# Performance work log

Measured on AMD Instinct MI355X. Metric: run time of the kernel, lower is better.

Reference implementation:

```python
import jax, jax.numpy as jnp
import numpy as np

N = 100000      # nodes
E = 1600000     # edges
G = 2048        # graphs
IN_DIM = 32
PEP_DIM = 768
H = 64          # hidden_dim
L = 3           # num_layers
BN_EPS = 1e-5


def setup_inputs() -> dict:
    key = jax.random.key(0)
    ks = jax.random.split(key, 32)
    x = jax.random.normal(ks[0], (N, IN_DIM), dtype=jnp.float32)
    edge_index = jax.random.randint(ks[1], (2, E), 0, N, dtype=jnp.int32)
    batch_idx = jnp.sort(jax.random.randint(ks[2], (N,), 0, G, dtype=jnp.int32))
    edge_attr = jax.random.normal(ks[3], (E, 2), dtype=jnp.float32)
    peptide_emb = jax.random.normal(ks[4], (G, PEP_DIM), dtype=jnp.float32)
    s = 0.1
    p = {
        'in_w': jax.random.normal(ks[5], (IN_DIM, H)) * s,
        'in_b': jnp.zeros((H,)),
        'e_w': jax.random.normal(ks[6], (2, H)) * s,
        'e_b': jnp.zeros((H,)),
        'conv_w1': jax.random.normal(ks[7], (L, H, H)) * s,
        'conv_b1': jnp.zeros((L, H)),
        'conv_w2': jax.random.normal(ks[8], (L, H, H)) * s,
        'conv_b2': jnp.zeros((L, H)),
        'bn_w': jnp.ones((L, H)),
        'bn_b': jnp.zeros((L, H)),
        'bn_mean': jnp.zeros((L, H)),
        'bn_var': jnp.ones((L, H)),
        'vn_w1': jax.random.normal(ks[9], (H, H)) * s,
        'vn_b1': jnp.zeros((H,)),
        'vn_w2': jax.random.normal(ks[10], (H, H)) * s,
        'vn_b2': jnp.zeros((H,)),
        'pep_w': jax.random.normal(ks[11], (PEP_DIM, H)) * s,
        'pep_b': jnp.zeros((H,)),
        'cls_w1': jax.random.normal(ks[12], (2 * H, H)) * s,
        'cls_b1': jnp.zeros((H,)),
        'cls_w2': jax.random.normal(ks[13], (H, 1)) * s,
        'cls_b2': jnp.zeros((1,)),
    }
    out = {'x': x, 'edge_index': edge_index, 'batch_idx': batch_idx,
           'edge_attr': edge_attr, 'peptide_emb': peptide_emb}
    out.update(p)
    return out


def reference(x, edge_index, batch_idx, edge_attr, peptide_emb,
              in_w, in_b, e_w, e_b,
              conv_w1, conv_b1, conv_w2, conv_b2,
              bn_w, bn_b, bn_mean, bn_var,
              vn_w1, vn_b1, vn_w2, vn_b2,
              pep_w, pep_b, cls_w1, cls_b1, cls_w2, cls_b2):
    seg = jax.ops.segment_sum
    src, dst = edge_index[0], edge_index[1]

    h = x @ in_w + in_b                       # [N,H]
    e = edge_attr @ e_w + e_b                 # [E,H]
    vn = jnp.zeros((G, H), dtype=h.dtype)     # virtual node per graph

    for i in range(L):
        h = h + vn[batch_idx]
        # GINE conv: (1+eps)*h + sum_j relu(h_j + e_ji), eps=0
        msg = jax.nn.relu(h[src] + e)                 # [E,H]
        agg = seg(msg, dst, num_segments=N)           # scatter-add to targets
        z = h + agg
        m = jax.nn.relu(z @ conv_w1[i] + conv_b1[i]) @ conv_w2[i] + conv_b2[i]
        # BatchNorm (eval: running stats)
        m = (m - bn_mean[i]) * jax.lax.rsqrt(bn_var[i] + BN_EPS) * bn_w[i] + bn_b[i]
        h = jax.nn.relu(m)                            # dropout = identity (eval)
        if i != L - 1:
            pooled = seg(h, batch_idx, num_segments=G)
            vn = vn + (jax.nn.relu(pooled @ vn_w1 + vn_b1) @ vn_w2 + vn_b2)

    # mean pooling
    counts = seg(jnp.ones((N,), dtype=h.dtype), batch_idx, num_segments=G)
    graph_emb = seg(h, batch_idx, num_segments=G) / jnp.maximum(counts, 1.0)[:, None]

    pep_hidden = jax.nn.relu(peptide_emb @ pep_w + pep_b)  # dropout = identity
    fused = jnp.concatenate([graph_emb, pep_hidden], axis=1)  # [G,2H]
    logits = (jax.nn.relu(fused @ cls_w1 + cls_b1) @ cls_w2 + cls_b2).reshape(-1)
    return logits
```

## Files before the change

kernel.cpp:

```cpp
#include <hip/hip_runtime.h>

#define NN 100000
#define NE 1600000
#define NG 2048
#define IN_DIM 32
#define PEP_DIM 768
#define H 64
#define BN_EPS 1e-5f
#define CONV_W 16
#define NGRP (NN / CONV_W)
#define GATHER_BLOCKS 512
#define NTILE ((NN + 63) / 64)
#define MLP_BLOCKS 512
#define BUCK_SHIFT 9
#define NBUCK ((NN + 511) >> 9)
#define NBLKA 256
#define CHUNK ((NE + NBLKA - 1) / NBLKA)

typedef unsigned int uint;
typedef unsigned short ushort;
typedef __attribute__((ext_vector_type(8))) __bf16 bf16x8;
typedef __attribute__((ext_vector_type(4))) float f32x4;

__device__ __forceinline__ float bf2f(uint u) {
    return __uint_as_float((u & 0xFFFFu) << 16);
}
__device__ __forceinline__ uint f2bf(float x) {
    uint b = __float_as_uint(x);
    return (b + 0x7FFFu + ((b >> 16) & 1u)) >> 16;
}


__global__ __launch_bounds__(256) void k_hist(const int* __restrict__ ei, int* __restrict__ mat) {
    __shared__ int hloc[NBUCK];
    for (int i = threadIdx.x; i < NBUCK; i += 256) hloc[i] = 0;
    __syncthreads();
    int base = blockIdx.x * CHUNK;
    int end = min(NE, base + CHUNK);
    for (int e = base + threadIdx.x; e < end; e += 256)
        atomicAdd(&hloc[ei[NE + e] >> BUCK_SHIFT], 1);
    __syncthreads();
    for (int i = threadIdx.x; i < NBUCK; i += 256)
        mat[i * NBLKA + blockIdx.x] = hloc[i];
}

__global__ __launch_bounds__(NBLKA) void k_s1(int* __restrict__ mat, int* __restrict__ tot) {
    __shared__ int s[NBLKA];
    int b = blockIdx.x;
    int v = mat[b * NBLKA + threadIdx.x];
    s[threadIdx.x] = v;
    __syncthreads();
    for (int off = 1; off < NBLKA; off <<= 1) {
        int x = (threadIdx.x >= off) ? s[threadIdx.x - off] : 0;
        __syncthreads();
        s[threadIdx.x] += x;
        __syncthreads();
    }
    mat[b * NBLKA + threadIdx.x] = s[threadIdx.x] - v;
    if (threadIdx.x == NBLKA - 1) tot[b] = s[threadIdx.x];
}

__global__ __launch_bounds__(256) void k_s2(const int* __restrict__ tot, int* __restrict__ bases) {
    __shared__ int s[256];
    int v = (threadIdx.x < NBUCK) ? tot[threadIdx.x] : 0;
    s[threadIdx.x] = v;
    __syncthreads();
    for (int off = 1; off < 256; off <<= 1) {
        int x = (threadIdx.x >= off) ? s[threadIdx.x - off] : 0;
        __syncthreads();
        s[threadIdx.x] += x;
        __syncthreads();
    }
    if (threadIdx.x < NBUCK) bases[threadIdx.x] = s[threadIdx.x] - v;
    if (threadIdx.x == 255) bases[NBUCK] = s[255];
}

__global__ __launch_bounds__(256) void k_scat1(const int* __restrict__ ei, const float* __restrict__ ea,
                                               const int* __restrict__ mat, const int* __restrict__ bases,
                                               int2* __restrict__ tmp) {
    __shared__ int cur[NBUCK];
    for (int i = threadIdx.x; i < NBUCK; i += 256)
        cur[i] = bases[i] + mat[i * NBLKA + blockIdx.x];
    __syncthreads();
    int base = blockIdx.x * CHUNK;
    int end = min(NE, base + CHUNK);
    for (int e = base + threadIdx.x; e < end; e += 256) {
        int dst = ei[NE + e];
        int bk = dst >> BUCK_SHIFT;
        int pos = atomicAdd(&cur[bk], 1);
        float2 a = *(const float2*)(ea + (size_t)e * 2);
        int2 r;
        r.x = ei[e] | ((dst & 511) << 17);
        r.y = (int)(f2bf(a.x) | (f2bf(a.y) << 16));
        tmp[pos] = r;
    }
}

__global__ __launch_bounds__(256) void k_scat2(const int2* __restrict__ tmp, const int* __restrict__ bases,
                                               int2* __restrict__ csr, int* __restrict__ row_start) {
    __shared__ int deg[512];
    __shared__ int psc[256];
    __shared__ int cur[512];
    int b = blockIdx.x;
    int t = threadIdx.x;
    int s0 = bases[b], s1 = bases[b + 1];
    deg[2 * t] = 0; deg[2 * t + 1] = 0;
    __syncthreads();
    for (int e = s0 + t; e < s1; e += 256)
        atomicAdd(&deg[(tmp[e].x >> 17) & 511], 1);
    __syncthreads();
    int d0 = deg[2 * t], d1 = deg[2 * t + 1];
    psc[t] = d0 + d1;
    __syncthreads();
    for (int off = 1; off < 256; off <<= 1) {
        int x = (t >= off) ? psc[t - off] : 0;
        __syncthreads();
        psc[t] += x;
        __syncthreads();
    }
    int ep = psc[t] - (d0 + d1);
    int node0 = (b << BUCK_SHIFT) + 2 * t;
    int e0 = s0 + ep, e1 = e0 + d0;
    cur[2 * t] = e0; cur[2 * t + 1] = e1;
    if (node0 < NN) row_start[node0] = e0;
    if (node0 + 1 < NN) row_start[node0 + 1] = e1;
    __syncthreads();
    for (int e = s0 + t; e < s1; e += 256) {
        int2 r = tmp[e];
        int nl = (r.x >> 17) & 511;
        int pos = atomicAdd(&cur[nl], 1);
        int2 o;
        o.x = r.x & 0x1FFFF;
        o.y = r.y;
        csr[pos] = o;
    }
    if (b == NBUCK - 1 && t == 0) row_start[NN] = NE;
}

__global__ void k_gstart(const int* __restrict__ batch, int* __restrict__ gstart) {
    int i = blockIdx.x * 256 + threadIdx.x;
    if (i >= NN) return;
    int b = batch[i];
    int p = (i == 0) ? -1 : batch[i - 1];
    for (int g = p + 1; g <= b; g++) gstart[g] = i;
    if (i == NN - 1) {
        for (int g = b + 1; g <= NG; g++) gstart[g] = NN;
    }
}

__global__ void k_init_h(const float* __restrict__ x, const float* __restrict__ w,
                         const float* __restrict__ b, ushort* __restrict__ h) {
    int t = blockIdx.x * 256 + threadIdx.x;
    int node = t >> 4;
    if (node >= NN) return;
    int c4 = (t & 15) * 4;
    float4 acc = *(const float4*)(b + c4);
    const float* xr = x + node * IN_DIM;
    for (int k = 0; k < IN_DIM; k++) {
        float xv = xr[k];
        float4 wv = *(const float4*)(w + k * H + c4);
        acc.x += xv * wv.x; acc.y += xv * wv.y;
        acc.z += xv * wv.z; acc.w += xv * wv.w;
    }
    uint2 o;
    o.x = f2bf(acc.x) | (f2bf(acc.y) << 16);
    o.y = f2bf(acc.z) | (f2bf(acc.w) << 16);
    *(uint2*)(h + (size_t)node * H + c4) = o;
}

__global__ void k_prep(const float* __restrict__ w1, const float* __restrict__ w2,
                       ushort* __restrict__ wp) {
    int t = blockIdx.x * 256 + threadIdx.x;
    if (t >= 3 * 8192) return;
    int j = t & 7;
    int lane = (t >> 3) & 63;
    int ct = (t >> 9) & 3;
    int ks = (t >> 11) & 1;
    int st = (t >> 12) & 1;
    int ly = t >> 13;
    int k = ks * 32 + (lane >> 4) * 8 + j;
    int c = ct * 16 + (lane & 15);
    const float* src = (st == 0) ? w1 : w2;
    wp[t] = (ushort)f2bf(src[ly * H * H + k * H + c]);
}

__global__ __launch_bounds__(1024, 4) void k_gather(
    const ushort* __restrict__ h_in, ushort* __restrict__ z,
    const int2* __restrict__ csr, const int* __restrict__ row_start,
    const float* __restrict__ ew, const float* __restrict__ eb) {
    int w = threadIdx.x >> 6;
    int c = threadIdx.x & 63;
    float ew0 = ew[c], ew1 = ew[H + c], ebc = eb[c];
    for (int grp = blockIdx.x; grp < NGRP; grp += GATHER_BLOCKS) {
        int node = grp * CONV_W + w;
        int rs = __builtin_amdgcn_readfirstlane(row_start[node]);
        int re = __builtin_amdgcn_readfirstlane(row_start[node + 1]);
        float acc = 0.f;
        int j = rs;
        for (; j + 16 <= re; j += 16) {
            int2 v[16];
            #pragma unroll
            for (int t = 0; t < 16; t++) v[t] = csr[j + t];
            float hh[16];
            #pragma unroll
            for (int t = 0; t < 16; t++) hh[t] = bf2f(h_in[(size_t)v[t].x * H + c]);
            #pragma unroll
            for (int t = 0; t < 16; t++)
                acc += fmaxf(hh[t] + fmaf(bf2f(v[t].y), ew0, fmaf(bf2f((uint)v[t].y >> 16), ew1, ebc)), 0.f);
        }
        for (; j + 4 <= re; j += 4) {
            int2 v[4];
            #pragma unroll
            for (int t = 0; t < 4; t++) v[t] = csr[j + t];
            float hh[4];
            #pragma unroll
            for (int t = 0; t < 4; t++) hh[t] = bf2f(h_in[(size_t)v[t].x * H + c]);
            #pragma unroll
            for (int t = 0; t < 4; t++)
                acc += fmaxf(hh[t] + fmaf(bf2f(v[t].y), ew0, fmaf(bf2f((uint)v[t].y >> 16), ew1, ebc)), 0.f);
        }
        for (; j < re; j++) {
            int2 v = csr[j];
            float hs = bf2f(h_in[(size_t)v.x * H + c]);
            acc += fmaxf(hs + fmaf(bf2f(v.y), ew0, fmaf(bf2f((uint)v.y >> 16), ew1, ebc)), 0.f);
        }
        float zv = bf2f(h_in[(size_t)node * H + c]) + acc;
        uint me = f2bf(zv);
        uint nb2 = __shfl_down(me, 1, 64);
        if ((c & 1) == 0) {
            *(uint*)(z + (size_t)node * H + c) = me | (nb2 << 16);
        }
    }
}

__global__ __launch_bounds__(256, 4) void k_mlp(
    const ushort* __restrict__ z, ushort* __restrict__ h_out,
    const ushort* __restrict__ wp,
    const float* __restrict__ b1, const float* __restrict__ b2,
    const float* __restrict__ bnw, const float* __restrict__ bnb,
    const float* __restrict__ bnm, const float* __restrict__ bnv) {
    __shared__ ushort ts[4][16][72];
    int w = threadIdx.x >> 6;
    int l = threadIdx.x & 63;
    int r = l & 15;
    int kg = l >> 4;
    bf16x8 W1B0[4], W1B1[4], W2B0[4], W2B1[4];
    #pragma unroll
    for (int ct = 0; ct < 4; ct++) {
        W1B0[ct] = *(const bf16x8*)(wp + (0 * 4 + ct) * 512 + l * 8);
        W1B1[ct] = *(const bf16x8*)(wp + (1 * 4 + ct) * 512 + l * 8);
        W2B0[ct] = *(const bf16x8*)(wp + 4096 + (0 * 4 + ct) * 512 + l * 8);
        W2B1[ct] = *(const bf16x8*)(wp + 4096 + (1 * 4 + ct) * 512 + l * 8);
    }
    for (int tile = blockIdx.x; tile < NTILE; tile += MLP_BLOCKS) {
        int nb = tile * 64 + w * 16;
        if (nb >= NN) continue;
        const ushort* zr = z + (size_t)(nb + r) * H + kg * 8;
        bf16x8 A0 = *(const bf16x8*)(zr);
        bf16x8 A1 = *(const bf16x8*)(zr + 32);
        f32x4 acc[4];
        #pragma unroll
        for (int ct = 0; ct < 4; ct++) {
            f32x4 a = {0.f, 0.f, 0.f, 0.f};
            a = __builtin_amdgcn_mfma_f32_16x16x32_bf16(A0, W1B0[ct], a, 0, 0, 0);
            a = __builtin_amdgcn_mfma_f32_16x16x32_bf16(A1, W1B1[ct], a, 0, 0, 0);
            acc[ct] = a;
        }
        #pragma unroll
        for (int ct = 0; ct < 4; ct++) {
            int col = ct * 16 + r;
            float bb = b1[col];
            #pragma unroll
            for (int q = 0; q < 4; q++) {
                float tv = fmaxf(acc[ct][q] + bb, 0.f);
                ts[w][kg * 4 + q][col] = (ushort)f2bf(tv);
            }
        }
        bf16x8 T0 = *(const bf16x8*)(&ts[w][r][kg * 8]);
        bf16x8 T1 = *(const bf16x8*)(&ts[w][r][32 + kg * 8]);
        f32x4 acc2[4];
        #pragma unroll
        for (int ct = 0; ct < 4; ct++) {
            f32x4 a = {0.f, 0.f, 0.f, 0.f};
            a = __builtin_amdgcn_mfma_f32_16x16x32_bf16(T0, W2B0[ct], a, 0, 0, 0);
            a = __builtin_amdgcn_mfma_f32_16x16x32_bf16(T1, W2B1[ct], a, 0, 0, 0);
            acc2[ct] = a;
        }
        #pragma unroll
        for (int ct = 0; ct < 4; ct++) {
            int col = ct * 16 + r;
            float bb2 = b2[col];
            float mean = bnm[col];
            float sc = bnw[col] * rsqrtf(bnv[col] + BN_EPS);
            float bo = bnb[col];
            #pragma unroll
            for (int q = 0; q < 4; q++) {
                float hv = fmaxf((acc2[ct][q] + bb2 - mean) * sc + bo, 0.f);
                ts[w][kg * 4 + q][col] = (ushort)f2bf(hv);
            }
        }
        #pragma unroll
        for (int it = 0; it < 4; it++) {
            int flat = it * 64 + l;
            int node = flat >> 4;
            int ch4 = (flat & 15) * 4;
            uint2 val = *(uint2*)(&ts[w][node][ch4]);
            *(uint2*)(h_out + (size_t)(nb + node) * H + ch4) = val;
        }
    }
}

__global__ __launch_bounds__(256) void k_poolvn(ushort* __restrict__ h,
                                                const int* __restrict__ gstart,
                                                float* __restrict__ pooled,
                                                const float* __restrict__ w1, const float* __restrict__ b1,
                                                const float* __restrict__ w2, const float* __restrict__ b2,
                                                float* __restrict__ vn, int do_vn) {
    __shared__ float ps[4][H];
    __shared__ float ts[4][H];
    int w = threadIdx.x >> 6, c = threadIdx.x & 63;
    int g = blockIdx.x * 4 + w;
    int s = __builtin_amdgcn_readfirstlane(gstart[g]);
    int e = __builtin_amdgcn_readfirstlane(gstart[g + 1]);
    float acc = 0.f;
    int n = s;
    for (; n + 4 <= e; n += 4) {
        float x0 = bf2f(h[(size_t)(n + 0) * H + c]);
        float x1 = bf2f(h[(size_t)(n + 1) * H + c]);
        float x2 = bf2f(h[(size_t)(n + 2) * H + c]);
        float x3 = bf2f(h[(size_t)(n + 3) * H + c]);
        acc += x0; acc += x1; acc += x2; acc += x3;
    }
    for (; n < e; n++) acc += bf2f(h[(size_t)n * H + c]);
    pooled[(size_t)g * H + c] = acc;
    if (!do_vn) return;
    ps[w][c] = acc;
    float a1 = b1[c];
    for (int k = 0; k < H; k += 4) {
        float4 pv = *(const float4*)&ps[w][k];
        a1 = fmaf(pv.x, w1[(k + 0) * H + c], a1);
        a1 = fmaf(pv.y, w1[(k + 1) * H + c], a1);
        a1 = fmaf(pv.z, w1[(k + 2) * H + c], a1);
        a1 = fmaf(pv.w, w1[(k + 3) * H + c], a1);
    }
    ts[w][c] = fmaxf(a1, 0.f);
    float a2 = b2[c];
    for (int k = 0; k < H; k += 4) {
        float4 tv = *(const float4*)&ts[w][k];
        a2 = fmaf(tv.x, w2[(k + 0) * H + c], a2);
        a2 = fmaf(tv.y, w2[(k + 1) * H + c], a2);
        a2 = fmaf(tv.z, w2[(k + 2) * H + c], a2);
        a2 = fmaf(tv.w, w2[(k + 3) * H + c], a2);
    }
    float vnew = vn[(size_t)g * H + c] + a2;
    vn[(size_t)g * H + c] = vnew;
    ps[w][c] = vnew;
    float vlo = ps[w][(c & 31) * 2 + 0];
    float vhi = ps[w][(c & 31) * 2 + 1];
    int ch2 = (c & 31) * 2;
    for (n = s; n + 2 <= e; n += 2) {
        size_t off = (size_t)(n + (c >> 5)) * H + ch2;
        uint u = *(uint*)(h + off);
        float lo = bf2f(u) + vlo;
        float hi = bf2f(u >> 16) + vhi;
        *(uint*)(h + off) = f2bf(lo) | (f2bf(hi) << 16);
    }
    if (n < e && c < 32) {
        size_t off = (size_t)n * H + ch2;
        uint u = *(uint*)(h + off);
        float lo = bf2f(u) + vlo;
        float hi = bf2f(u >> 16) + vhi;
        *(uint*)(h + off) = f2bf(lo) | (f2bf(hi) << 16);
    }
}

__global__ __launch_bounds__(256) void k_final(const float* __restrict__ pooled,
                                               const int* __restrict__ gstart,
                                               const float* __restrict__ pep,
                                               const float* __restrict__ pw, const float* __restrict__ pb,
                                               const float* __restrict__ cw1, const float* __restrict__ cb1,
                                               const float* __restrict__ cw2, const float* __restrict__ cb2,
                                               float* __restrict__ out) {
    __shared__ float red[4][H];
    __shared__ float fused[2 * H];
    int g = blockIdx.x;
    int lane = threadIdx.x & 63;
    int part = threadIdx.x >> 6;
    const float* pr = pep + (size_t)g * PEP_DIM;
    float acc = 0.0f;
    int k0 = part * (PEP_DIM / 4);
    for (int k = k0; k < k0 + PEP_DIM / 4; k++) {
        acc += pr[k] * pw[k * H + lane];
    }
    red[part][lane] = acc;
    __syncthreads();
    if (part == 0) {
        float s = red[0][lane] + red[1][lane] + red[2][lane] + red[3][lane] + pb[lane];
        fused[H + lane] = fmaxf(s, 0.0f);
        float c = (float)(gstart[g + 1] - gstart[g]);
        float invc = 1.0f / fmaxf(c, 1.0f);
        fused[lane] = pooled[(size_t)g * H + lane] * invc;
    }
    __syncthreads();
    if (part == 0) {
        float a = cb1[lane];
        for (int k = 0; k < 2 * H; k++) a += fused[k] * cw1[k * H + lane];
        float t = fmaxf(a, 0.0f);
        float v = t * cw2[lane];
        for (int off = 32; off > 0; off >>= 1) v += __shfl_down(v, off, 64);
        if (lane == 0) out[g] = v + cb2[0];
    }
}

extern "C" void kernel_launch(void* const* d_in, const int* in_sizes, int n_in,
                              void* d_out, int out_size, void* d_ws, size_t ws_size,
                              hipStream_t stream) {
    const float* x        = (const float*)d_in[0];
    const int*   ei       = (const int*)d_in[1];
    const int*   batch    = (const int*)d_in[2];
    const float* ea       = (const float*)d_in[3];
    const float* pep      = (const float*)d_in[4];
    const float* in_w     = (const float*)d_in[5];
    const float* in_b     = (const float*)d_in[6];
    const float* e_w      = (const float*)d_in[7];
    const float* e_b      = (const float*)d_in[8];
    const float* conv_w1  = (const float*)d_in[9];
    const float* conv_b1  = (const float*)d_in[10];
    const float* conv_w2  = (const float*)d_in[11];
    const float* conv_b2  = (const float*)d_in[12];
    const float* bn_w     = (const float*)d_in[13];
    const float* bn_b     = (const float*)d_in[14];
    const float* bn_mean  = (const float*)d_in[15];
    const float* bn_var   = (const float*)d_in[16];
    const float* vn_w1    = (const float*)d_in[17];
    const float* vn_b1    = (const float*)d_in[18];
    const float* vn_w2    = (const float*)d_in[19];
    const float* vn_b2    = (const float*)d_in[20];
    const float* pep_w    = (const float*)d_in[21];
    const float* pep_b    = (const float*)d_in[22];
    const float* cls_w1   = (const float*)d_in[23];
    const float* cls_b1   = (const float*)d_in[24];
    const float* cls_w2   = (const float*)d_in[25];
    const float* cls_b2   = (const float*)d_in[26];
    float* out = (float*)d_out;

    ushort* h_a   = (ushort*)d_ws;
    ushort* h_b   = h_a + (size_t)NN * H;
    ushort* z     = h_b + (size_t)NN * H;
    int2*  tmp    = (int2*)z;
    float* pooled = (float*)(z + (size_t)NN * H);
    float* vn     = pooled + (size_t)NG * H;
    int2*  csr    = (int2*)(vn + (size_t)NG * H);
    ushort* wp    = (ushort*)(csr + (size_t)NE);
    int* row_start = (int*)(wp + 3 * 8192);
    int* gstart    = row_start + NN + 16;
    int* mat       = gstart + NG + 16;
    int* tot       = mat + NBUCK * NBLKA;
    int* bases     = tot + NBUCK;

    k_hist<<<NBLKA, 256, 0, stream>>>(ei, mat);
    k_s1<<<NBUCK, NBLKA, 0, stream>>>(mat, tot);
    k_s2<<<1, 256, 0, stream>>>(tot, bases);
    k_scat1<<<NBLKA, 256, 0, stream>>>(ei, ea, mat, bases, tmp);
    k_scat2<<<NBUCK, 256, 0, stream>>>(tmp, bases, csr, row_start);
    k_gstart<<<(NN + 255) / 256, 256, 0, stream>>>(batch, gstart);
    k_prep<<<(3 * 8192 + 255) / 256, 256, 0, stream>>>(conv_w1, conv_w2, wp);

    k_init_h<<<NN * 16 / 256, 256, 0, stream>>>(x, in_w, in_b, h_a);
    hipMemsetAsync(vn, 0, (size_t)NG * H * sizeof(float), stream);

    ushort* hc = h_a;
    ushort* hn = h_b;
    for (int i = 0; i < 3; i++) {
        k_gather<<<GATHER_BLOCKS, 1024, 0, stream>>>(hc, z, csr, row_start, e_w, e_b);
        k_mlp<<<MLP_BLOCKS, 256, 0, stream>>>(z, hn, wp + i * 8192,
                                              conv_b1 + i * H, conv_b2 + i * H,
                                              bn_w + i * H, bn_b + i * H,
                                              bn_mean + i * H, bn_var + i * H);
        ushort* t = hc; hc = hn; hn = t;
        k_poolvn<<<NG / 4, 256, 0, stream>>>(hc, gstart, pooled,
                                             vn_w1, vn_b1, vn_w2, vn_b2, vn,
                                             (i < 2) ? 1 : 0);
    }

    k_final<<<NG, 256, 0, stream>>>(pooled, gstart, pep, pep_w, pep_b,
                                    cls_w1, cls_b1, cls_w2, cls_b2, out);
}
```

Baseline: 313.5 us.

## Fold virtual-node broadcast into edge gather instead of rewriting h in place

Each node's graph id is packed into the upper bits of the CSR source field. The gather kernel then adds the virtual-node vector on the fly, for each gathered neighbour and for the self term. This removes the read-modify-write pass over the whole node feature array that k_poolvn did to apply vn each layer. The cost is an extra fp32 vn load per edge in the latency-bound gather loop, plus some bit unpacking. The vn add also now happens in fp32 rather than being rounded into bf16 h.

Result: slower. 339.7 us (+8.4%).

```diff
diff --git a/kernel.cpp b/kernel.cpp
--- a/kernel.cpp
+++ b/kernel.cpp
@@ -97,6 +97,7 @@
 }
 
 __global__ __launch_bounds__(256) void k_scat2(const int2* __restrict__ tmp, const int* __restrict__ bases,
+                                               const int* __restrict__ batch,
                                                int2* __restrict__ csr, int* __restrict__ row_start) {
     __shared__ int deg[512];
     __shared__ int psc[256];
@@ -129,8 +130,10 @@
         int2 r = tmp[e];
         int nl = (r.x >> 17) & 511;
         int pos = atomicAdd(&cur[nl], 1);
+        int src = r.x & 0x1FFFF;
+        int bid = batch[src];
         int2 o;
-        o.x = r.x & 0x1FFFF;
+        o.x = src | (bid << 17);
         o.y = r.y;
         csr[pos] = o;
     }
@@ -187,6 +190,7 @@
 __global__ __launch_bounds__(1024, 4) void k_gather(
     const ushort* __restrict__ h_in, ushort* __restrict__ z,
     const int2* __restrict__ csr, const int* __restrict__ row_start,
+    const float* __restrict__ vn, const int* __restrict__ batch,
     const float* __restrict__ ew, const float* __restrict__ eb) {
     int w = threadIdx.x >> 6;
     int c = threadIdx.x & 63;
@@ -201,30 +205,43 @@
             int2 v[16];
             #pragma unroll
             for (int t = 0; t < 16; t++) v[t] = csr[j + t];
-            float hh[16];
-            #pragma unroll
-            for (int t = 0; t < 16; t++) hh[t] = bf2f(h_in[(size_t)v[t].x * H + c]);
+            float hh[16], vv[16];
+            #pragma unroll
+            for (int t = 0; t < 16; t++) {
+                uint src = (uint)v[t].x & 0x1FFFFu;
+                uint bid = (uint)v[t].x >> 17;
+                hh[t] = bf2f(h_in[(size_t)src * H + c]);
+                vv[t] = vn[(size_t)bid * H + c];
+            }
             #pragma unroll
             for (int t = 0; t < 16; t++)
-                acc += fmaxf(hh[t] + fmaf(bf2f(v[t].y), ew0, fmaf(bf2f((uint)v[t].y >> 16), ew1, ebc)), 0.f);
+                acc += fmaxf(hh[t] + vv[t] + fmaf(bf2f(v[t].y), ew0, fmaf(bf2f((uint)v[t].y >> 16), ew1, ebc)), 0.f);
         }
         for (; j + 4 <= re; j += 4) {
             int2 v[4];
             #pragma unroll
             for (int t = 0; t < 4; t++) v[t] = csr[j + t];
-            float hh[4];
-            #pragma unroll
-            for (int t = 0; t < 4; t++) hh[t] = bf2f(h_in[(size_t)v[t].x * H + c]);
+            float hh[4], vv[4];
+            #pragma unroll
+            for (int t = 0; t < 4; t++) {
+                uint src = (uint)v[t].x & 0x1FFFFu;
+                uint bid = (uint)v[t].x >> 17;
+                hh[t] = bf2f(h_in[(size_t)src * H + c]);
+                vv[t] = vn[(size_t)bid * H + c];
+            }
             #pragma unroll
             for (int t = 0; t < 4; t++)
-                acc += fmaxf(hh[t] + fmaf(bf2f(v[t].y), ew0, fmaf(bf2f((uint)v[t].y >> 16), ew1, ebc)), 0.f);
+                acc += fmaxf(hh[t] + vv[t] + fmaf(bf2f(v[t].y), ew0, fmaf(bf2f((uint)v[t].y >> 16), ew1, ebc)), 0.f);
         }
         for (; j < re; j++) {
             int2 v = csr[j];
-            float hs = bf2f(h_in[(size_t)v.x * H + c]);
+            uint src = (uint)v.x & 0x1FFFFu;
+            uint bid = (uint)v.x >> 17;
+            float hs = bf2f(h_in[(size_t)src * H + c]) + vn[(size_t)bid * H + c];
             acc += fmaxf(hs + fmaf(bf2f(v.y), ew0, fmaf(bf2f((uint)v.y >> 16), ew1, ebc)), 0.f);
         }
-        float zv = bf2f(h_in[(size_t)node * H + c]) + acc;
+        int bidn = __builtin_amdgcn_readfirstlane(batch[node]);
+        float zv = bf2f(h_in[(size_t)node * H + c]) + vn[(size_t)bidn * H + c] + acc;
         uint me = f2bf(zv);
         uint nb2 = __shfl_down(me, 1, 64);
         if ((c & 1) == 0) {
@@ -310,7 +327,7 @@
     }
 }
 
-__global__ __launch_bounds__(256) void k_poolvn(ushort* __restrict__ h,
+__global__ __launch_bounds__(256) void k_poolvn(const ushort* __restrict__ h,
                                                 const int* __restrict__ gstart,
                                                 float* __restrict__ pooled,
                                                 const float* __restrict__ w1, const float* __restrict__ b1,
@@ -352,26 +369,7 @@
         a2 = fmaf(tv.z, w2[(k + 2) * H + c], a2);
         a2 = fmaf(tv.w, w2[(k + 3) * H + c], a2);
     }
-    float vnew = vn[(size_t)g * H + c] + a2;
-    vn[(size_t)g * H + c] = vnew;
-    ps[w][c] = vnew;
-    float vlo = ps[w][(c & 31) * 2 + 0];
-    float vhi = ps[w][(c & 31) * 2 + 1];
-    int ch2 = (c & 31) * 2;
-    for (n = s; n + 2 <= e; n += 2) {
-        size_t off = (size_t)(n + (c >> 5)) * H + ch2;
-        uint u = *(uint*)(h + off);
-        float lo = bf2f(u) + vlo;
-        float hi = bf2f(u >> 16) + vhi;
-        *(uint*)(h + off) = f2bf(lo) | (f2bf(hi) << 16);
-    }
-    if (n < e && c < 32) {
-        size_t off = (size_t)n * H + ch2;
-        uint u = *(uint*)(h + off);
-        float lo = bf2f(u) + vlo;
-        float hi = bf2f(u >> 16) + vhi;
-        *(uint*)(h + off) = f2bf(lo) | (f2bf(hi) << 16);
-    }
+    vn[(size_t)g * H + c] += a2;
 }
 
 __global__ __launch_bounds__(256) void k_final(const float* __restrict__ pooled,
@@ -462,7 +460,7 @@
     k_s1<<<NBUCK, NBLKA, 0, stream>>>(mat, tot);
     k_s2<<<1, 256, 0, stream>>>(tot, bases);
     k_scat1<<<NBLKA, 256, 0, stream>>>(ei, ea, mat, bases, tmp);
-    k_scat2<<<NBUCK, 256, 0, stream>>>(tmp, bases, csr, row_start);
+    k_scat2<<<NBUCK, 256, 0, stream>>>(tmp, bases, batch, csr, row_start);
     k_gstart<<<(NN + 255) / 256, 256, 0, stream>>>(batch, gstart);
     k_prep<<<(3 * 8192 + 255) / 256, 256, 0, stream>>>(conv_w1, conv_w2, wp);
 
@@ -472,7 +470,7 @@
     ushort* hc = h_a;
     ushort* hn = h_b;
     for (int i = 0; i < 3; i++) {
-        k_gather<<<GATHER_BLOCKS, 1024, 0, stream>>>(hc, z, csr, row_start, e_w, e_b);
+        k_gather<<<GATHER_BLOCKS, 1024, 0, stream>>>(hc, z, csr, row_start, vn, batch, e_w, e_b);
         k_mlp<<<MLP_BLOCKS, 256, 0, stream>>>(z, hn, wp + i * 8192,
                                               conv_b1 + i * H, conv_b2 + i * H,
                                               bn_w + i * H, bn_b + i * H,
```
